# Optimization experiments

Hardware: AMD Instinct MI355X
Metric: run time of the kernel (lower is better)

## Reference

```python
import jax, jax.numpy as jnp
import numpy as np

N, T, F_IN = 20000, 13, 3
E = 320000
NB, NL = 4, 2
C_RES, C_DIL, C_SKIP, C_END = 32, 32, 256, 512
KSZ, KHOP = 2, 4
N_PRED, N_OUT = 12, 2
L = NB * NL
DILS = [2 ** i for _ in range(NB) for i in range(NL)]  # [1,2,1,2,1,2,1,2]
EPS = 1e-5


def _dconv(x, w, d):
    # x: [N,C,T], w: [O,I,K]; valid dilated conv -> [N,O,T-(K-1)*d]
    return jax.lax.conv_general_dilated(x, w, (1,), 'VALID', rhs_dilation=(d,),
                                        dimension_numbers=('NCH', 'OIH', 'NCH'))


def _forward(inputs, edge_src, edge_dst, enter_w, enter_b, filt_w, filt_b, gate_w, gate_b,
             gc_w, gc_b, skip_w, skip_b, bn_g, bn_b, out1_w, out1_b, out2_w, out2_b):
    # inputs: [N,T,F] -> x: [N,C_RES,T] via 1x1 conv (enter)
    x = jnp.einsum('of,ntf->not', enter_w, inputs) + enter_b[None, :, None]
    deg = jax.ops.segment_sum(jnp.ones((E,), x.dtype), edge_dst, num_segments=N)
    deg = jnp.maximum(deg, 1.0)[:, None, None]

    def propagate(h):  # [N,t,C]: mean over incoming edges (normalized diffusion step)
        return jax.ops.segment_sum(h[edge_src], edge_dst, num_segments=N) / deg

    skip = jnp.zeros((N, C_SKIP, T), x.dtype)
    for l in range(L):
        d = DILS[l]
        f = jnp.tanh(_dconv(x, filt_w[l], d) + filt_b[l][None, :, None])
        g = jax.nn.sigmoid(_dconv(x, gate_w[l], d) + gate_b[l][None, :, None])
        h = f * g                                   # [N,C_DIL,t]
        t = h.shape[-1]
        skip = skip[..., -t:] + jnp.einsum('oc,nct->not', skip_w[l], h) + skip_b[l][None, :, None]
        # K-hop graph diffusion conv on [N,t,C]
        hh = h.transpose(0, 2, 1)
        acc = jnp.einsum('ntc,co->nto', hh, gc_w[l, 0])
        cur = hh
        for k in range(1, KHOP):
            cur = propagate(cur)
            acc = acc + jnp.einsum('ntc,co->nto', cur, gc_w[l, k])
        acc = acc + gc_b[l]
        x = acc.transpose(0, 2, 1) + x[..., -t:]    # residual add
        # BatchNorm1d over (N, t) per channel (training-mode batch stats)
        mu = x.mean(axis=(0, 2), keepdims=True)
        var = x.var(axis=(0, 2), keepdims=True)
        x = bn_g[l][None, :, None] * (x - mu) * jax.lax.rsqrt(var + EPS) + bn_b[l][None, :, None]
    y = jax.nn.relu(skip)                           # [N,C_SKIP,1]
    y = jax.nn.relu(jnp.einsum('oc,nct->not', out1_w, y) + out1_b[None, :, None])
    y = jnp.einsum('oc,nct->not', out2_w, y) + out2_b[None, :, None]  # [N,n_pred*n_out,1]
    return y.reshape(N, N_PRED, -1)


def setup_inputs() -> dict:
    key = jax.random.key(0)
    ks = jax.random.split(key, 12)
    s = 0.05
    f32 = jnp.float32
    return {
        'inputs': jax.random.normal(ks[0], (N, T, F_IN), f32),
        'edge_src': jax.random.randint(ks[1], (E,), 0, N),
        'edge_dst': jax.random.randint(ks[2], (E,), 0, N),
        'enter_w': jax.random.normal(ks[3], (C_RES, F_IN), f32) * s,
        'enter_b': jnp.zeros((C_RES,), f32),
        'filt_w': jax.random.normal(ks[4], (L, C_DIL, C_RES, KSZ), f32) * s,
        'filt_b': jnp.zeros((L, C_DIL), f32),
        'gate_w': jax.random.normal(ks[5], (L, C_DIL, C_RES, KSZ), f32) * s,
        'gate_b': jnp.zeros((L, C_DIL), f32),
        'gc_w': jax.random.normal(ks[6], (L, KHOP, C_DIL, C_RES), f32) * s,
        'gc_b': jnp.zeros((L, C_RES), f32),
        'skip_w': jax.random.normal(ks[7], (L, C_SKIP, C_DIL), f32) * s,
        'skip_b': jnp.zeros((L, C_SKIP), f32),
        'bn_g': jnp.ones((L, C_RES), f32),
        'bn_b': jnp.zeros((L, C_RES), f32),
        'out1_w': jax.random.normal(ks[8], (C_END, C_SKIP), f32) * s,
        'out1_b': jnp.zeros((C_END,), f32),
        'out2_w': jax.random.normal(ks[9], (N_PRED * N_OUT, C_END), f32) * s,
        'out2_b': jnp.zeros((N_PRED * N_OUT,), f32),
    }


def reference(inputs, edge_src, edge_dst, enter_w, enter_b, filt_w, filt_b, gate_w, gate_b,
              gc_w, gc_b, skip_w, skip_b, bn_g, bn_b, out1_w, out1_b, out2_w, out2_b):
    return _forward(inputs, edge_src, edge_dst, enter_w, enter_b, filt_w, filt_b, gate_w, gate_b,
                    gc_w, gc_b, skip_w, skip_b, bn_g, bn_b, out1_w, out1_b, out2_w, out2_b)
```

## Files before the change

kernel.cpp:

```cpp
#include <hip/hip_runtime.h>
#include <cmath>

constexpr int N = 20000, T = 13, E = 320000;
constexpr int NB_SCAN = (N + 255) / 256;
constexpr int NPART = 64;
typedef unsigned int uint32;

typedef __attribute__((ext_vector_type(8))) short short8;
typedef __attribute__((ext_vector_type(4))) float f32x4;

__device__ __forceinline__ unsigned short f2bf(float f) {
  unsigned int u = __float_as_uint(f);
  unsigned int r = (u + 0x7FFFu + ((u >> 16) & 1u)) >> 16;
  return (unsigned short)r;
}
__device__ __forceinline__ float bflo(uint32 v) { return __uint_as_float(v << 16); }
__device__ __forceinline__ float bfhi(uint32 v) { return __uint_as_float(v & 0xFFFF0000u); }
__device__ __forceinline__ uint32 packbf(float lo, float hi) {
  return (uint32)f2bf(lo) | ((uint32)f2bf(hi) << 16);
}

constexpr size_t WALIGN = 512;
constexpr size_t align_up(size_t x) { return (x + WALIGN - 1) & ~(WALIGN - 1); }

constexpr size_t XA_OFF  = 0;
constexpr size_t X_SZ    = align_up((size_t)N * 13 * 32 * 4);
constexpr size_t XB_OFF  = XA_OFF + X_SZ;
constexpr size_t H_OFF   = XB_OFF + X_SZ;
constexpr size_t H_SZ    = align_up((size_t)N * 12 * 32 * 4);
constexpr size_t C1_OFF  = H_OFF + H_SZ;
constexpr size_t C2_OFF  = C1_OFF + H_SZ;
constexpr size_t C3_OFF  = C2_OFF + H_SZ;
constexpr size_t HL_OFF  = C3_OFF + H_SZ;
constexpr size_t HL_SZ   = align_up((size_t)N * 256 * 4);
constexpr size_t WS2_OFF = HL_OFF + HL_SZ;
constexpr size_t SB_OFF  = WS2_OFF + align_up(256 * 256 * 4);
constexpr size_t SUMS_OFF = SB_OFF + align_up(256 * 4);
constexpr size_t PAR_OFF  = SUMS_OFF + align_up(8 * NPART * 64 * 4);
constexpr size_t CNT_OFF  = PAR_OFF + align_up(9 * 64 * 4);
constexpr size_t ROW_OFF  = CNT_OFF + align_up((size_t)N * 4);
constexpr size_t FILL_OFF = ROW_OFF + align_up((size_t)(N + 1) * 4);
constexpr size_t COL_OFF  = FILL_OFF + align_up((size_t)N * 4);
constexpr size_t DEG_OFF  = COL_OFF + align_up((size_t)E * 4);
constexpr size_t BP_OFF   = DEG_OFF + align_up((size_t)N * 4);
constexpr size_t CP_OFF   = BP_OFF + align_up(8 * 2048 * 4);
constexpr size_t BW1_OFF  = CP_OFF + align_up(8 * 2176 * 4);
constexpr size_t BW2_OFF  = BW1_OFF + align_up(32768 * 4);
constexpr size_t BS_OFF   = BW2_OFF + align_up(65536 * 4);
constexpr size_t BO_OFF   = BS_OFF + align_up((size_t)NB_SCAN * 4);
constexpr size_t S_OFF  = C2_OFF;
constexpr size_t Y1_OFF = H_OFF;

__global__ void k_count(const int* __restrict__ dst, int* __restrict__ cnt) {
  int i = blockIdx.x * 256 + threadIdx.x;
  if (i < E) atomicAdd(&cnt[dst[i]], 1);
}

__global__ __launch_bounds__(256) void k_scan1(const int* __restrict__ cnt, int* __restrict__ bsum) {
  __shared__ int sc[256];
  int t = threadIdx.x; int idx = blockIdx.x * 256 + t;
  int v = (idx < N) ? cnt[idx] : 0;
  sc[t] = v; __syncthreads();
  for (int off = 1; off < 256; off <<= 1) {
    int u = (t >= off) ? sc[t - off] : 0;
    __syncthreads();
    sc[t] += u;
    __syncthreads();
  }
  if (t == 255) bsum[blockIdx.x] = sc[255];
}

__global__ __launch_bounds__(256) void k_scan2(const int* __restrict__ bsum, int* __restrict__ boff) {
  __shared__ int sc[256];
  int t = threadIdx.x;
  int v = (t < NB_SCAN) ? bsum[t] : 0;
  sc[t] = v; __syncthreads();
  for (int off = 1; off < 256; off <<= 1) {
    int u = (t >= off) ? sc[t - off] : 0;
    __syncthreads();
    sc[t] += u;
    __syncthreads();
  }
  if (t < NB_SCAN) boff[t] = sc[t] - v;
  if (t == 255) boff[NB_SCAN] = sc[255];
}

__global__ __launch_bounds__(256) void k_scan3(const int* __restrict__ cnt, const int* __restrict__ boff,
                                               int* __restrict__ rowptr, int* __restrict__ fill,
                                               float* __restrict__ deginv) {
  __shared__ int sc[256];
  int t = threadIdx.x; int idx = blockIdx.x * 256 + t;
  int v = (idx < N) ? cnt[idx] : 0;
  sc[t] = v; __syncthreads();
  for (int off = 1; off < 256; off <<= 1) {
    int u = (t >= off) ? sc[t - off] : 0;
    __syncthreads();
    sc[t] += u;
    __syncthreads();
  }
  if (idx < N) {
    int run = boff[blockIdx.x] + sc[t] - v;
    rowptr[idx] = run; fill[idx] = run;
    deginv[idx] = 1.0f / (float)(v > 1 ? v : 1);
  }
  if (blockIdx.x == 0 && t == 0) rowptr[N] = boff[NB_SCAN];
}

__global__ void k_scatter(const int* __restrict__ src, const int* __restrict__ dst,
                          int* __restrict__ fill, int* __restrict__ col) {
  int i = blockIdx.x * 256 + threadIdx.x;
  if (i < E) { int d = dst[i]; int p = atomicAdd(&fill[d], 1); col[p] = src[i]; }
}

__global__ void k_init_params(float* __restrict__ par) {
  int i = threadIdx.x;
  par[i] = (i < 32) ? 1.0f : 0.0f;
}

__global__ void k_prep_gcw(const float* __restrict__ gcw, uint32* __restrict__ bp) {
  int idx = blockIdx.x * 256 + threadIdx.x;
  if (idx >= 8 * 4 * 2 * 64 * 4) return;
  int w4 = idx & 3, lane = (idx >> 2) & 63, hh = (idx >> 8) & 1, s = (idx >> 9) & 3, l = idx >> 11;
  int n = lane & 15, q = lane >> 4;
  int k0 = q * 8 + w4 * 2, o = hh * 16 + n;
  const float* g = gcw + (((size_t)(l * 4 + s) * 32 + k0) * 32 + o);
  bp[idx] = packbf(g[0], g[32]);
}

__global__ void k_prep_bw(const float* __restrict__ W, uint32* __restrict__ bp, int O) {
  int idx = blockIdx.x * 256 + threadIdx.x;
  int total = (O / 16) * 8 * 64 * 4;
  if (idx >= total) return;
  int w4 = idx & 3, lane = (idx >> 2) & 63, ks = (idx >> 8) & 7, ot = idx >> 11;
  int n = lane & 15, q = lane >> 4;
  int k = ks * 32 + q * 8 + w4 * 2;
  const float* wr = W + (size_t)(ot * 16 + n) * 256 + k;
  bp[idx] = packbf(wr[0], wr[1]);
}

__global__ void k_prep_conv(const float* __restrict__ fw, const float* __restrict__ fb,
                            const float* __restrict__ gw, const float* __restrict__ gb,
                            const float* __restrict__ par, int layer, uint32* __restrict__ cpbuf) {
  uint32* base = cpbuf + (size_t)layer * 2176;
  int tid = blockIdx.x * 256 + threadIdx.x;
  if (tid < 2048) {
    int w4 = tid & 3, lane = (tid >> 2) & 63, hh = (tid >> 8) & 1, ktap = (tid >> 9) & 1, sel = tid >> 10;
    int n = lane & 15, q = lane >> 4;
    int c0 = q * 8 + w4 * 2, o = hh * 16 + n;
    const float* w = sel ? gw : fw;
    float sc0 = par[layer * 64 + c0], sc1 = par[layer * 64 + c0 + 1];
    float v0 = w[(((size_t)layer * 32 + o) * 32 + c0) * 2 + ktap] * sc0;
    float v1 = w[(((size_t)layer * 32 + o) * 32 + c0 + 1) * 2 + ktap] * sc1;
    base[tid] = packbf(v0, v1);
  } else if (tid < 2048 + 64) {
    int i = tid - 2048; int sel = i >> 5; int o = i & 31;
    const float* w = sel ? gw : fw;
    const float* b = sel ? gb : fb;
    float s = b[layer * 32 + o];
    for (int c = 0; c < 32; c++) {
      float sh = par[layer * 64 + 32 + c];
      s += (w[(((size_t)layer * 32 + o) * 32 + c) * 2 + 0] +
            w[(((size_t)layer * 32 + o) * 32 + c) * 2 + 1]) * sh;
    }
    ((float*)base)[2048 + i] = s;
  }
}

__global__ void k_enter(const float* __restrict__ in, const float* __restrict__ w,
                        const float* __restrict__ b, uint32* __restrict__ x) {
  int idx = blockIdx.x * 256 + threadIdx.x;
  if (idx >= N * 13 * 16) return;
  int cw = idx & 15; int tmp = idx >> 4; int t = tmp % 13; int n = tmp / 13;
  int c0 = cw * 2;
  const float* ip = in + (size_t)n * (13 * 3) + t * 3;
  float v0 = b[c0]     + w[c0 * 3 + 0]       * ip[0] + w[c0 * 3 + 1]       * ip[1] + w[c0 * 3 + 2]       * ip[2];
  float v1 = b[c0 + 1] + w[(c0 + 1) * 3 + 0] * ip[0] + w[(c0 + 1) * 3 + 1] * ip[1] + w[(c0 + 1) * 3 + 2] * ip[2];
  x[idx] = packbf(v0, v1);
}

template <int TIN, int TOUT, int D>
__global__ __launch_bounds__(256, 4) void k_conv(const uint32* __restrict__ x,
    const uint32* __restrict__ cpbuf, int layer,
    uint32* __restrict__ h, float* __restrict__ hlast) {
  constexpr int RS = 34;
  __shared__ float xst[128 * RS];
  int tid = threadIdx.x;
  int wave = tid >> 6, lane = tid & 63;
  int m = lane & 15, q = lane >> 4;
  int nrows = N * TOUT;
  int base = blockIdx.x * 128;

  const uint32* cp = cpbuf + (size_t)layer * 2176;
  short8 bf[2][2][2];
#pragma unroll
  for (int sel = 0; sel < 2; sel++)
#pragma unroll
    for (int kt = 0; kt < 2; kt++)
#pragma unroll
      for (int hh = 0; hh < 2; hh++)
        bf[sel][kt][hh] = *(const short8*)(cp + (size_t)(((sel * 2 + kt) * 2 + hh) * 64 + lane) * 4);
  const float* bias = (const float*)(cp + 2048);
  float fb0 = bias[m], fb1 = bias[16 + m], gb0 = bias[32 + m], gb1 = bias[48 + m];

#pragma unroll
  for (int tile = 0; tile < 2; tile++) {
    int row = base + wave * 32 + tile * 16 + m;
    bool valid = row < nrows;
    int rr = valid ? row : 0;
    int n = rr / TOUT, tt = rr - n * TOUT;
    const uint32* xr = x + ((size_t)n * TIN + tt) * 16 + q * 4;
    short8 a0 = {0,0,0,0,0,0,0,0}, aD = {0,0,0,0,0,0,0,0};
    if (valid) { a0 = *(const short8*)xr; aD = *(const short8*)(xr + D * 16); }
    f32x4 aF0 = {0.f,0.f,0.f,0.f}, aF1 = {0.f,0.f,0.f,0.f};
    f32x4 aG0 = {0.f,0.f,0.f,0.f}, aG1 = {0.f,0.f,0.f,0.f};
    aF0 = __builtin_amdgcn_mfma_f32_16x16x32_bf16(a0, bf[0][0][0], aF0, 0, 0, 0);
    aF0 = __builtin_amdgcn_mfma_f32_16x16x32_bf16(aD, bf[0][1][0], aF0, 0, 0, 0);
    aF1 = __builtin_amdgcn_mfma_f32_16x16x32_bf16(a0, bf[0][0][1], aF1, 0, 0, 0);
    aF1 = __builtin_amdgcn_mfma_f32_16x16x32_bf16(aD, bf[0][1][1], aF1, 0, 0, 0);
    aG0 = __builtin_amdgcn_mfma_f32_16x16x32_bf16(a0, bf[1][0][0], aG0, 0, 0, 0);
    aG0 = __builtin_amdgcn_mfma_f32_16x16x32_bf16(aD, bf[1][1][0], aG0, 0, 0, 0);
    aG1 = __builtin_amdgcn_mfma_f32_16x16x32_bf16(a0, bf[1][0][1], aG1, 0, 0, 0);
    aG1 = __builtin_amdgcn_mfma_f32_16x16x32_bf16(aD, bf[1][1][1], aG1, 0, 0, 0);
#pragma unroll
    for (int r = 0; r < 4; r++) {
      int lrow = wave * 32 + tile * 16 + q * 4 + r;
      float F0 = aF0[r] + fb0, G0 = aG0[r] + gb0;
      float F1 = aF1[r] + fb1, G1 = aG1[r] + gb1;
      float af0 = fabsf(F0), ef0 = __expf(-2.0f * af0);
      float th0 = copysignf((1.0f - ef0) / (1.0f + ef0), F0);
      float hv0 = th0 * (1.0f / (1.0f + __expf(-G0)));
      float af1 = fabsf(F1), ef1 = __expf(-2.0f * af1);
      float th1 = copysignf((1.0f - ef1) / (1.0f + ef1), F1);
      float hv1 = th1 * (1.0f / (1.0f + __expf(-G1)));
      xst[lrow * RS + m]      = hv0;
      xst[lrow * RS + 16 + m] = hv1;
    }
  }
  __syncthreads();
  {
    uint2* outp = (uint2*)h;
#pragma unroll
    for (int it = 0; it < 4; it++) {
      int l = it * 256 + tid;
      int g = base * 8 + l;
      if (g < nrows * 8) {
        int rl = l >> 3, j4 = l & 7;
        float2 a = *(const float2*)&xst[rl * RS + j4 * 4];
        float2 b = *(const float2*)&xst[rl * RS + j4 * 4 + 2];
        outp[g] = make_uint2(packbf(a.x, a.y), packbf(b.x, b.y));
        int grow = base + rl;
        int node = grow / TOUT, tt = grow - node * TOUT;
        if (tt == TOUT - 1) {
          *(float4*)(hlast + (size_t)node * 256 + layer * 32 + j4 * 4) = make_float4(a.x, a.y, b.x, b.y);
        }
      }
    }
  }
}

template <int F>
__global__ __launch_bounds__(256) void k_hop(const uint32* __restrict__ in, uint32* __restrict__ out,
    const int* __restrict__ rowptr, const int* __restrict__ col, const float* __restrict__ deginv) {
  constexpr int F2 = F / 2;
  constexpr int NW = (F2 + 63) / 64;
  int wid = (blockIdx.x * 256 + threadIdx.x) >> 6;
  int lane = threadIdx.x & 63;
  if (wid >= N) return;
  int s = rowptr[wid], e = rowptr[wid + 1];
  float alo[NW], ahi[NW];
#pragma unroll
  for (int k = 0; k < NW; k++) { alo[k] = 0.0f; ahi[k] = 0.0f; }
  int idx = s;
  for (; idx + 7 < e; idx += 8) {
    const uint32* p[8];
#pragma unroll
    for (int q = 0; q < 8; q++) p[q] = in + (size_t)col[idx + q] * F2;
    uint32 v[8][NW];
#pragma unroll
    for (int q = 0; q < 8; q++) {
#pragma unroll
      for (int k = 0; k < NW; k++) {
        int j = k * 64 + lane;
        v[q][k] = (j < F2) ? p[q][j] : 0u;
      }
    }
#pragma unroll
    for (int k = 0; k < NW; k++) {
      alo[k] += ((bflo(v[0][k]) + bflo(v[1][k])) + (bflo(v[2][k]) + bflo(v[3][k]))) +
                ((bflo(v[4][k]) + bflo(v[5][k])) + (bflo(v[6][k]) + bflo(v[7][k])));
      ahi[k] += ((bfhi(v[0][k]) + bfhi(v[1][k])) + (bfhi(v[2][k]) + bfhi(v[3][k]))) +
                ((bfhi(v[4][k]) + bfhi(v[5][k])) + (bfhi(v[6][k]) + bfhi(v[7][k])));
    }
  }
  for (; idx + 3 < e; idx += 4) {
    const uint32* p0 = in + (size_t)col[idx] * F2;
    const uint32* p1 = in + (size_t)col[idx + 1] * F2;
    const uint32* p2 = in + (size_t)col[idx + 2] * F2;
    const uint32* p3 = in + (size_t)col[idx + 3] * F2;
#pragma unroll
    for (int k = 0; k < NW; k++) {
      int j = k * 64 + lane;
      if (j < F2) {
        uint32 v0 = p0[j], v1 = p1[j], v2 = p2[j], v3 = p3[j];
        alo[k] += (bflo(v0) + bflo(v1)) + (bflo(v2) + bflo(v3));
        ahi[k] += (bfhi(v0) + bfhi(v1)) + (bfhi(v2) + bfhi(v3));
      }
    }
  }
  for (; idx < e; ++idx) {
    const uint32* p = in + (size_t)col[idx] * F2;
#pragma unroll
    for (int k = 0; k < NW; k++) {
      int j = k * 64 + lane;
      if (j < F2) { uint32 v = p[j]; alo[k] += bflo(v); ahi[k] += bfhi(v); }
    }
  }
  float inv = deginv[wid];
  uint32* q = out + (size_t)wid * F2;
#pragma unroll
  for (int k = 0; k < NW; k++) {
    int j = k * 64 + lane;
    if (j < F2) q[j] = packbf(alo[k] * inv, ahi[k] * inv);
  }
}

template <int TIN, int TOUT>
__global__ __launch_bounds__(256, 4) void k_combine(const uint32* __restrict__ h,
    const uint32* __restrict__ c1, const uint32* __restrict__ c2, const uint32* __restrict__ c3,
    const uint32* __restrict__ bpack, const float* __restrict__ gcb,
    const uint32* __restrict__ xcur, int layer,
    const float* __restrict__ par, int slot,
    uint32* __restrict__ xnext, float* __restrict__ sums) {
  constexpr int RS = 34;
  __shared__ float xst[128 * RS];
  __shared__ float pbuf[96];
  __shared__ float r1s[32], r2s[32];
  int tid = threadIdx.x;
  if (tid < 32) {
    pbuf[tid]      = gcb[layer * 32 + tid];
    pbuf[32 + tid] = par[slot * 64 + tid];
    pbuf[64 + tid] = par[slot * 64 + 32 + tid];
    r1s[tid] = 0.0f; r2s[tid] = 0.0f;
  }

  int nrows = N * TOUT;
  int base = blockIdx.x * 128;
  int wave = tid >> 6, lane = tid & 63;
  int m = lane & 15, q = lane >> 4;

  const uint32* bp = bpack + (size_t)layer * 2048;
  short8 bf[4][2];
#pragma unroll
  for (int s = 0; s < 4; s++)
#pragma unroll
    for (int hh = 0; hh < 2; hh++)
      bf[s][hh] = *(const short8*)(bp + (size_t)((s * 2 + hh) * 64 + lane) * 4);

  f32x4 acc[2][2] = {{{0.f,0.f,0.f,0.f},{0.f,0.f,0.f,0.f}},{{0.f,0.f,0.f,0.f},{0.f,0.f,0.f,0.f}}};
  const uint32* srcs[4] = { h, c1, c2, c3 };
#pragma unroll
  for (int s = 0; s < 4; s++) {
    const uint32* sp = srcs[s];
#pragma unroll
    for (int t = 0; t < 2; t++) {
      int row = base + wave * 32 + t * 16 + m;
      short8 af = {0,0,0,0,0,0,0,0};
      if (row < nrows) af = *(const short8*)(sp + (size_t)row * 16 + q * 4);
      acc[t][0] = __builtin_amdgcn_mfma_f32_16x16x32_bf16(af, bf[s][0], acc[t][0], 0, 0, 0);
      acc[t][1] = __builtin_amdgcn_mfma_f32_16x16x32_bf16(af, bf[s][1], acc[t][1], 0, 0, 0);
    }
  }

  __syncthreads();
#pragma unroll
  for (int t = 0; t < 2; t++)
#pragma unroll
    for (int hh = 0; hh < 2; hh++)
#pragma unroll
      for (int r = 0; r < 4; r++)
        xst[(wave * 32 + t * 16 + q * 4 + r) * RS + hh * 16 + m] = acc[t][hh][r];
  __syncthreads();

  constexpr int toff = TIN - TOUT;
  int rg = tid >> 3, oq = tid & 7;
  float gb0 = pbuf[oq * 4 + 0], gb1 = pbuf[oq * 4 + 1], gb2 = pbuf[oq * 4 + 2], gb3 = pbuf[oq * 4 + 3];
  float sc0 = pbuf[32 + oq * 4 + 0], sc1 = pbuf[32 + oq * 4 + 1], sc2 = pbuf[32 + oq * 4 + 2], sc3 = pbuf[32 + oq * 4 + 3];
  float sh0 = pbuf[64 + oq * 4 + 0], sh1 = pbuf[64 + oq * 4 + 1], sh2 = pbuf[64 + oq * 4 + 2], sh3 = pbuf[64 + oq * 4 + 3];
  float s1[4] = {0.f, 0.f, 0.f, 0.f}, s2[4] = {0.f, 0.f, 0.f, 0.f};
#pragma unroll
  for (int i = 0; i < 4; i++) {
    int r = rg + 32 * i;
    int row = base + r;
    bool act = row < nrows;
    float2 aa = *(const float2*)&xst[r * RS + oq * 4];
    float2 ab = *(const float2*)&xst[r * RS + oq * 4 + 2];
    float xr0 = 0.f, xr1 = 0.f, xr2 = 0.f, xr3 = 0.f;
    if (act) {
      int node = row / TOUT, t_ = row - node * TOUT;
      const uint32* rp = xcur + ((size_t)node * TIN + toff + t_) * 16 + oq * 2;
      uint32 va = rp[0], vb = rp[1];
      xr0 = bflo(va); xr1 = bfhi(va); xr2 = bflo(vb); xr3 = bfhi(vb);
    }
    float v0 = aa.x + gb0 + sc0 * xr0 + sh0;
    float v1 = aa.y + gb1 + sc1 * xr1 + sh1;
    float v2 = ab.x + gb2 + sc2 * xr2 + sh2;
    float v3 = ab.y + gb3 + sc3 * xr3 + sh3;
    *(float2*)&xst[r * RS + oq * 4]     = make_float2(v0, v1);
    *(float2*)&xst[r * RS + oq * 4 + 2] = make_float2(v2, v3);
    if (act) {
      s1[0] += v0; s1[1] += v1; s1[2] += v2; s1[3] += v3;
      s2[0] += v0 * v0; s2[1] += v1 * v1; s2[2] += v2 * v2; s2[3] += v3 * v3;
    }
  }
#pragma unroll
  for (int j = 0; j < 4; j++) {
    atomicAdd(&r1s[oq * 4 + j], s1[j]);
    atomicAdd(&r2s[oq * 4 + j], s2[j]);
  }
  __syncthreads();

  {
    uint2* outp = (uint2*)xnext;
#pragma unroll
    for (int it = 0; it < 4; it++) {
      int l = it * 256 + tid;
      int g = base * 8 + l;
      if (g < nrows * 8) {
        int rl = l >> 3, j4 = l & 7;
        float2 a = *(const float2*)&xst[rl * RS + j4 * 4];
        float2 b = *(const float2*)&xst[rl * RS + j4 * 4 + 2];
        outp[g] = make_uint2(packbf(a.x, a.y), packbf(b.x, b.y));
      }
    }
  }
  {
    int part = blockIdx.x & (NPART - 1);
    float* sp = sums + ((size_t)layer * NPART + part) * 64;
    if (tid < 32) atomicAdd(&sp[tid], r1s[tid]);
    else if (tid < 64) atomicAdd(&sp[tid], r2s[tid - 32]);
  }
}

__global__ void k_bnfin(const float* __restrict__ sums, const float* __restrict__ bng,
                        const float* __restrict__ bnb, float* __restrict__ par,
                        int layer, int tout) {
  int o = threadIdx.x;
  float cnt = (float)N * (float)tout;
  float s1 = 0.0f, s2 = 0.0f;
  const float* lp = sums + (size_t)layer * NPART * 64;
  for (int p = 0; p < NPART; p++) {
    s1 += lp[p * 64 + o];
    s2 += lp[p * 64 + 32 + o];
  }
  float mu = s1 / cnt;
  float var = s2 / cnt - mu * mu;
  float sc = bng[layer * 32 + o] * rsqrtf(var + 1e-5f);
  par[(layer + 1) * 64 + o] = sc;
  par[(layer + 1) * 64 + 32 + o] = bnb[layer * 32 + o] - mu * sc;
}

__global__ void k_prep_skipw(const float* __restrict__ sw, float* __restrict__ w2) {
  int idx = blockIdx.x * 256 + threadIdx.x;
  if (idx >= 8 * 256 * 32) return;
  int l = idx / (256 * 32), r = idx % (256 * 32), o = r / 32, c = r & 31;
  w2[o * 256 + l * 32 + c] = sw[idx];
}
__global__ void k_prep_sb(const float* __restrict__ sb, float* __restrict__ out) {
  int o = threadIdx.x;
  float s = 0.0f;
  for (int l = 0; l < 8; l++) s += sb[l * 256 + o];
  out[o] = s;
}

__global__ __launch_bounds__(256) void k_mgemm(const float* __restrict__ A, const uint32* __restrict__ bp,
    const float* __restrict__ bias, float* __restrict__ C, int M, int Onum, int relu) {
  constexpr int RS = 68;
  __shared__ float xst[128 * RS];
  int tid = threadIdx.x;
  int wave = tid >> 6, lane = tid & 63;
  int m = lane & 15, q = lane >> 4;
  int base = blockIdx.x * 128;
  int ot0 = blockIdx.y * 4;

  f32x4 acc[2][4];
#pragma unroll
  for (int t = 0; t < 2; t++)
#pragma unroll
    for (int nt = 0; nt < 4; nt++) acc[t][nt] = (f32x4){0.f, 0.f, 0.f, 0.f};

#pragma unroll 1
  for (int ks = 0; ks < 8; ks++) {
    short8 a[2];
#pragma unroll
    for (int t = 0; t < 2; t++) {
      int row = base + wave * 32 + t * 16 + m;
      float4 f0 = make_float4(0.f, 0.f, 0.f, 0.f), f1 = f0;
      if (row < M) {
        const float* ap = A + (size_t)row * 256 + ks * 32 + q * 8;
        f0 = *(const float4*)ap;
        f1 = *(const float4*)(ap + 4);
      }
      uint32 u[4];
      u[0] = packbf(f0.x, f0.y); u[1] = packbf(f0.z, f0.w);
      u[2] = packbf(f1.x, f1.y); u[3] = packbf(f1.z, f1.w);
      a[t] = *(const short8*)u;
    }
#pragma unroll
    for (int nt = 0; nt < 4; nt++) {
      short8 b = *(const short8*)(bp + (size_t)(((ot0 + nt) * 8 + ks) * 64 + lane) * 4);
      acc[0][nt] = __builtin_amdgcn_mfma_f32_16x16x32_bf16(a[0], b, acc[0][nt], 0, 0, 0);
      acc[1][nt] = __builtin_amdgcn_mfma_f32_16x16x32_bf16(a[1], b, acc[1][nt], 0, 0, 0);
    }
  }

#pragma unroll
  for (int t = 0; t < 2; t++)
#pragma unroll
    for (int nt = 0; nt < 4; nt++) {
      float bv = bias[blockIdx.y * 64 + nt * 16 + m];
#pragma unroll
      for (int r = 0; r < 4; r++) {
        float v = acc[t][nt][r] + bv;
        if (relu) v = fmaxf(v, 0.0f);
        xst[(wave * 32 + t * 16 + q * 4 + r) * RS + nt * 16 + m] = v;
      }
    }
  __syncthreads();

#pragma unroll
  for (int it = 0; it < 8; it++) {
    int l = it * 256 + tid;
    int rl = l >> 4, c4 = l & 15;
    int grow = base + rl;
    if (grow < M) {
      float4 v = *(const float4*)&xst[rl * RS + c4 * 4];
      *(float4*)(C + (size_t)grow * Onum + blockIdx.y * 64 + c4 * 4) = v;
    }
  }
}

__global__ __launch_bounds__(256) void k_final2(const float* __restrict__ Y1, const float* __restrict__ W2,
                                                const float* __restrict__ b2, float* __restrict__ out) {
  __shared__ float y1s[64][68];
  __shared__ float w2s[24][65];
  int tid = threadIdx.x;
  int bm = blockIdx.x * 64;
  int k0 = blockIdx.y * 64;
  for (int i = tid; i < 64 * 16; i += 256) {
    int r = i >> 4, k4 = i & 15;
    int gm = bm + r;
    float4 v = make_float4(0.f, 0.f, 0.f, 0.f);
    if (gm < N) v = *(const float4*)(Y1 + (size_t)gm * 512 + k0 + k4 * 4);
    y1s[r][k4 * 4 + 0] = v.x; y1s[r][k4 * 4 + 1] = v.y;
    y1s[r][k4 * 4 + 2] = v.z; y1s[r][k4 * 4 + 3] = v.w;
  }
  for (int i = tid; i < 24 * 16; i += 256) {
    int o = i >> 4, k4 = i & 15;
    float4 v = *(const float4*)(W2 + (size_t)o * 512 + k0 + k4 * 4);
    w2s[o][k4 * 4 + 0] = v.x; w2s[o][k4 * 4 + 1] = v.y;
    w2s[o][k4 * 4 + 2] = v.z; w2s[o][k4 * 4 + 3] = v.w;
  }
  __syncthreads();
  int rg = tid >> 5;
  int o = tid & 31;
  if (o < 24) {
    float acc[8] = {};
    for (int kk = 0; kk < 64; kk++) {
      float w = w2s[o][kk];
#pragma unroll
      for (int i = 0; i < 8; i++) acc[i] += y1s[rg * 8 + i][kk] * w;
    }
    float bias = (blockIdx.y == 0) ? b2[o] : 0.0f;
#pragma unroll
    for (int i = 0; i < 8; i++) {
      int gm = bm + rg * 8 + i;
      if (gm < N) atomicAdd(&out[(size_t)gm * 24 + o], acc[i] + bias);
    }
  }
}

struct Ptrs {
  const float *fw, *fb, *gw, *gb, *gcb, *bng, *bnb;
  const uint32 *bpack;
  uint32 *cpack;
  void *H, *C1, *C2, *C3;
  float *HL, *par, *sums;
  const int *row, *col;
  const float *deg;
};

template <int TIN, int TOUT, int D>
static void run_layer(int layer, bool last, const Ptrs& P, uint32*& xc, uint32*& xn, hipStream_t stream) {
  int cblocks = (N * TOUT + 127) / 128;
  k_conv<TIN, TOUT, D><<<cblocks, 256, 0, stream>>>(xc, P.cpack, layer, (uint32*)P.H, P.HL);
  if (!last) {
    constexpr int F = TOUT * 32;
    int hb = (N * 64 + 255) / 256;
    k_hop<F><<<hb, 256, 0, stream>>>((const uint32*)P.H, (uint32*)P.C1, P.row, P.col, P.deg);
    k_hop<F><<<hb, 256, 0, stream>>>((const uint32*)P.C1, (uint32*)P.C2, P.row, P.col, P.deg);
    k_hop<F><<<hb, 256, 0, stream>>>((const uint32*)P.C2, (uint32*)P.C3, P.row, P.col, P.deg);
    k_combine<TIN, TOUT><<<cblocks, 256, 0, stream>>>((const uint32*)P.H, (const uint32*)P.C1,
                                                      (const uint32*)P.C2, (const uint32*)P.C3,
                                                      P.bpack, P.gcb, xc, layer, P.par, layer, xn, P.sums);
    k_bnfin<<<1, 32, 0, stream>>>(P.sums, P.bng, P.bnb, P.par, layer, TOUT);
    k_prep_conv<<<9, 256, 0, stream>>>(P.fw, P.fb, P.gw, P.gb, P.par, layer + 1, P.cpack);
    uint32* tmp = xc; xc = xn; xn = tmp;
  }
}

extern "C" void kernel_launch(void* const* d_in, const int* in_sizes, int n_in,
                              void* d_out, int out_size, void* d_ws, size_t ws_size,
                              hipStream_t stream) {
  const float* inputs  = (const float*)d_in[0];
  const int*   esrc    = (const int*)d_in[1];
  const int*   edst    = (const int*)d_in[2];
  const float* enter_w = (const float*)d_in[3];
  const float* enter_b = (const float*)d_in[4];
  const float* filt_w  = (const float*)d_in[5];
  const float* filt_b  = (const float*)d_in[6];
  const float* gate_w  = (const float*)d_in[7];
  const float* gate_b  = (const float*)d_in[8];
  const float* gc_w    = (const float*)d_in[9];
  const float* gc_b    = (const float*)d_in[10];
  const float* skip_w  = (const float*)d_in[11];
  const float* skip_b  = (const float*)d_in[12];
  const float* bn_g    = (const float*)d_in[13];
  const float* bn_b    = (const float*)d_in[14];
  const float* out1_w  = (const float*)d_in[15];
  const float* out1_b  = (const float*)d_in[16];
  const float* out2_w  = (const float*)d_in[17];
  const float* out2_b  = (const float*)d_in[18];

  char* ws = (char*)d_ws;
  uint32* XA = (uint32*)(ws + XA_OFF);
  uint32* XB = (uint32*)(ws + XB_OFF);
  void* H    = (void*)(ws + H_OFF);
  void* C1   = (void*)(ws + C1_OFF);
  void* C2   = (void*)(ws + C2_OFF);
  void* C3   = (void*)(ws + C3_OFF);
  float* HL  = (float*)(ws + HL_OFF);
  float* WS2 = (float*)(ws + WS2_OFF);
  float* SB  = (float*)(ws + SB_OFF);
  float* SUMS = (float*)(ws + SUMS_OFF);
  float* PAR  = (float*)(ws + PAR_OFF);
  int* CNT  = (int*)(ws + CNT_OFF);
  int* ROW  = (int*)(ws + ROW_OFF);
  int* FILL = (int*)(ws + FILL_OFF);
  int* COL  = (int*)(ws + COL_OFF);
  float* DEG = (float*)(ws + DEG_OFF);
  uint32* BP = (uint32*)(ws + BP_OFF);
  uint32* CP = (uint32*)(ws + CP_OFF);
  uint32* BW1 = (uint32*)(ws + BW1_OFF);
  uint32* BW2 = (uint32*)(ws + BW2_OFF);
  int* BS = (int*)(ws + BS_OFF);
  int* BO = (int*)(ws + BO_OFF);
  float* S  = (float*)(ws + S_OFF);
  float* Y1 = (float*)(ws + Y1_OFF);

  hipMemsetAsync(CNT, 0, (size_t)N * 4, stream);
  hipMemsetAsync(SUMS, 0, (size_t)8 * NPART * 64 * 4, stream);
  hipMemsetAsync(d_out, 0, (size_t)out_size * 4, stream);

  k_count<<<(E + 255) / 256, 256, 0, stream>>>(edst, CNT);
  k_scan1<<<NB_SCAN, 256, 0, stream>>>(CNT, BS);
  k_scan2<<<1, 256, 0, stream>>>(BS, BO);
  k_scan3<<<NB_SCAN, 256, 0, stream>>>(CNT, BO, ROW, FILL, DEG);
  k_scatter<<<(E + 255) / 256, 256, 0, stream>>>(esrc, edst, FILL, COL);
  k_init_params<<<1, 64, 0, stream>>>(PAR);
  k_prep_gcw<<<(8 * 4 * 2 * 64 * 4 + 255) / 256, 256, 0, stream>>>(gc_w, BP);
  k_prep_conv<<<9, 256, 0, stream>>>(filt_w, filt_b, gate_w, gate_b, PAR, 0, CP);
  k_enter<<<(N * 13 * 16 + 255) / 256, 256, 0, stream>>>(inputs, enter_w, enter_b, XA);
  k_prep_skipw<<<(8 * 256 * 32 + 255) / 256, 256, 0, stream>>>(skip_w, WS2);
  k_prep_sb<<<1, 256, 0, stream>>>(skip_b, SB);
  k_prep_bw<<<(32768 + 255) / 256, 256, 0, stream>>>(WS2, BW1, 256);
  k_prep_bw<<<(65536 + 255) / 256, 256, 0, stream>>>(out1_w, BW2, 512);

  Ptrs P;
  P.fw = filt_w; P.fb = filt_b; P.gw = gate_w; P.gb = gate_b;
  P.gcb = gc_b; P.bng = bn_g; P.bnb = bn_b; P.bpack = BP; P.cpack = CP;
  P.H = H; P.C1 = C1; P.C2 = C2; P.C3 = C3; P.HL = HL; P.par = PAR; P.sums = SUMS;
  P.row = ROW; P.col = COL; P.deg = DEG;

  uint32* xc = XA; uint32* xn = XB;
  run_layer<13, 12, 1>(0, false, P, xc, xn, stream);
  run_layer<12, 10, 2>(1, false, P, xc, xn, stream);
  run_layer<10, 9, 1>(2, false, P, xc, xn, stream);
  run_layer<9, 7, 2>(3, false, P, xc, xn, stream);
  run_layer<7, 6, 1>(4, false, P, xc, xn, stream);
  run_layer<6, 4, 2>(5, false, P, xc, xn, stream);
  run_layer<4, 3, 1>(6, false, P, xc, xn, stream);
  run_layer<3, 1, 2>(7, true, P, xc, xn, stream);

  dim3 g1((N + 127) / 128, 4);
  k_mgemm<<<g1, 256, 0, stream>>>(HL, BW1, SB, S, N, 256, 1);
  dim3 g2((N + 127) / 128, 8);
  k_mgemm<<<g2, 256, 0, stream>>>(S, BW2, out1_b, Y1, N, 512, 1);
  dim3 gf((N + 63) / 64, 8);
  k_final2<<<gf, 256, 0, stream>>>(Y1, out2_w, out2_b, (float*)d_out);
}
```

Before: 1.018 ms.

## Fuse output head GEMMs with bf16 intermediates and MFMA final projection

Stores the last-step hidden features and the skip GEMM output in bf16 rather than fp32, so the A operands load directly as MFMA fragments without conversion. The second head GEMM is fused with the final 512->24 projection via MFMA on the ReLU'd tile in shared memory. This removes the fp32 Y1 intermediate and the separate scalar k_final2 kernel. Each block now computes 8 output tiles instead of 4, which raises register use, and the final outputs are still summed with atomics across column blocks.

```diff
diff --git a/kernel.cpp b/kernel.cpp
--- a/kernel.cpp
+++ b/kernel.cpp
@@ -49,7 +49,6 @@
 constexpr size_t BS_OFF   = BW2_OFF + align_up(65536 * 4);
 constexpr size_t BO_OFF   = BS_OFF + align_up((size_t)NB_SCAN * 4);
 constexpr size_t S_OFF  = C2_OFF;
-constexpr size_t Y1_OFF = H_OFF;
 
 __global__ void k_count(const int* __restrict__ dst, int* __restrict__ cnt) {
   int i = blockIdx.x * 256 + threadIdx.x;
@@ -136,6 +135,18 @@
   int k = ks * 32 + q * 8 + w4 * 2;
   const float* wr = W + (size_t)(ot * 16 + n) * 256 + k;
   bp[idx] = packbf(wr[0], wr[1]);
+}
+
+__global__ void k_prep_w2(const float* __restrict__ W, uint32* __restrict__ bp) {
+  int idx = blockIdx.x * 256 + threadIdx.x;
+  if (idx >= 2 * 16 * 64 * 4) return;
+  int w4 = idx & 3, lane = (idx >> 2) & 63, ks = (idx >> 8) & 15, ot = idx >> 12;
+  int n = lane & 15, q = lane >> 4;
+  int k = ks * 32 + q * 8 + w4 * 2;
+  int o = ot * 16 + n;
+  float v0 = 0.0f, v1 = 0.0f;
+  if (o < 24) { const float* wr = W + (size_t)o * 512 + k; v0 = wr[0]; v1 = wr[1]; }
+  bp[idx] = packbf(v0, v1);
 }
 
 __global__ void k_prep_conv(const float* __restrict__ fw, const float* __restrict__ fb,
@@ -181,7 +192,7 @@
 template <int TIN, int TOUT, int D>
 __global__ __launch_bounds__(256, 4) void k_conv(const uint32* __restrict__ x,
     const uint32* __restrict__ cpbuf, int layer,
-    uint32* __restrict__ h, float* __restrict__ hlast) {
+    uint32* __restrict__ h, uint32* __restrict__ hlast) {
   constexpr int RS = 34;
   __shared__ float xst[128 * RS];
   int tid = threadIdx.x;
@@ -247,11 +258,12 @@
         int rl = l >> 3, j4 = l & 7;
         float2 a = *(const float2*)&xst[rl * RS + j4 * 4];
         float2 b = *(const float2*)&xst[rl * RS + j4 * 4 + 2];
-        outp[g] = make_uint2(packbf(a.x, a.y), packbf(b.x, b.y));
+        uint2 pv = make_uint2(packbf(a.x, a.y), packbf(b.x, b.y));
+        outp[g] = pv;
         int grow = base + rl;
         int node = grow / TOUT, tt = grow - node * TOUT;
         if (tt == TOUT - 1) {
-          *(float4*)(hlast + (size_t)node * 256 + layer * 32 + j4 * 4) = make_float4(a.x, a.y, b.x, b.y);
+          *(uint2*)(hlast + (size_t)node * 128 + layer * 16 + j4 * 2) = pv;
         }
       }
     }
@@ -472,111 +484,160 @@
   out[o] = s;
 }
 
-__global__ __launch_bounds__(256) void k_mgemm(const float* __restrict__ A, const uint32* __restrict__ bp,
-    const float* __restrict__ bias, float* __restrict__ C, int M, int Onum, int relu) {
+__global__ __launch_bounds__(256) void k_gemm1(const uint32* __restrict__ A,
+    const uint32* __restrict__ bp, const float* __restrict__ bias, uint32* __restrict__ Sb) {
   constexpr int RS = 68;
   __shared__ float xst[128 * RS];
   int tid = threadIdx.x;
   int wave = tid >> 6, lane = tid & 63;
   int m = lane & 15, q = lane >> 4;
   int base = blockIdx.x * 128;
-  int ot0 = blockIdx.y * 4;
-
-  f32x4 acc[2][4];
+  int ot0 = blockIdx.y * 8;
+
+  f32x4 acc[2][8];
 #pragma unroll
   for (int t = 0; t < 2; t++)
 #pragma unroll
-    for (int nt = 0; nt < 4; nt++) acc[t][nt] = (f32x4){0.f, 0.f, 0.f, 0.f};
-
+    for (int nt = 0; nt < 8; nt++) acc[t][nt] = (f32x4){0.f, 0.f, 0.f, 0.f};
+
+  int row0 = base + wave * 32 + m;
+  int row1 = row0 + 16;
 #pragma unroll 1
   for (int ks = 0; ks < 8; ks++) {
-    short8 a[2];
-#pragma unroll
-    for (int t = 0; t < 2; t++) {
-      int row = base + wave * 32 + t * 16 + m;
-      float4 f0 = make_float4(0.f, 0.f, 0.f, 0.f), f1 = f0;
-      if (row < M) {
-        const float* ap = A + (size_t)row * 256 + ks * 32 + q * 8;
-        f0 = *(const float4*)ap;
-        f1 = *(const float4*)(ap + 4);
-      }
-      uint32 u[4];
-      u[0] = packbf(f0.x, f0.y); u[1] = packbf(f0.z, f0.w);
-      u[2] = packbf(f1.x, f1.y); u[3] = packbf(f1.z, f1.w);
-      a[t] = *(const short8*)u;
-    }
-#pragma unroll
-    for (int nt = 0; nt < 4; nt++) {
+    short8 a0 = {0,0,0,0,0,0,0,0}, a1 = {0,0,0,0,0,0,0,0};
+    if (row0 < N) a0 = *(const short8*)(A + (size_t)row0 * 128 + ks * 16 + q * 4);
+    if (row1 < N) a1 = *(const short8*)(A + (size_t)row1 * 128 + ks * 16 + q * 4);
+#pragma unroll
+    for (int nt = 0; nt < 8; nt++) {
       short8 b = *(const short8*)(bp + (size_t)(((ot0 + nt) * 8 + ks) * 64 + lane) * 4);
-      acc[0][nt] = __builtin_amdgcn_mfma_f32_16x16x32_bf16(a[0], b, acc[0][nt], 0, 0, 0);
-      acc[1][nt] = __builtin_amdgcn_mfma_f32_16x16x32_bf16(a[1], b, acc[1][nt], 0, 0, 0);
-    }
-  }
-
+      acc[0][nt] = __builtin_amdgcn_mfma_f32_16x16x32_bf16(a0, b, acc[0][nt], 0, 0, 0);
+      acc[1][nt] = __builtin_amdgcn_mfma_f32_16x16x32_bf16(a1, b, acc[1][nt], 0, 0, 0);
+    }
+  }
+
+#pragma unroll
+  for (int half = 0; half < 2; half++) {
+    if (half) __syncthreads();
+#pragma unroll
+    for (int t = 0; t < 2; t++)
+#pragma unroll
+      for (int nn = 0; nn < 4; nn++) {
+        float bv = bias[blockIdx.y * 128 + (half * 4 + nn) * 16 + m];
+#pragma unroll
+        for (int r = 0; r < 4; r++) {
+          float v = acc[t][half * 4 + nn][r] + bv;
+          xst[(wave * 32 + t * 16 + q * 4 + r) * RS + nn * 16 + m] = fmaxf(v, 0.0f);
+        }
+      }
+    __syncthreads();
+#pragma unroll
+    for (int it = 0; it < 8; it++) {
+      int l = it * 256 + tid;
+      int rl = l >> 4, c4 = l & 15;
+      int grow = base + rl;
+      if (grow < N) {
+        float2 a = *(const float2*)&xst[rl * RS + c4 * 4];
+        float2 b = *(const float2*)&xst[rl * RS + c4 * 4 + 2];
+        *(uint2*)(Sb + (size_t)grow * 128 + blockIdx.y * 64 + half * 32 + c4 * 2) =
+            make_uint2(packbf(a.x, a.y), packbf(b.x, b.y));
+      }
+    }
+  }
+}
+
+__global__ __launch_bounds__(256) void k_gemm2f(const uint32* __restrict__ A,
+    const uint32* __restrict__ bp, const float* __restrict__ bias,
+    const uint32* __restrict__ w2p, const float* __restrict__ b2, float* __restrict__ out) {
+  constexpr int RS = 68;
+  __shared__ float xst[128 * RS];
+  int tid = threadIdx.x;
+  int wave = tid >> 6, lane = tid & 63;
+  int m = lane & 15, q = lane >> 4;
+  int base = blockIdx.x * 128;
+  int ot0 = blockIdx.y * 8;
+
+  f32x4 acc[2][8];
 #pragma unroll
   for (int t = 0; t < 2; t++)
 #pragma unroll
-    for (int nt = 0; nt < 4; nt++) {
-      float bv = bias[blockIdx.y * 64 + nt * 16 + m];
-#pragma unroll
-      for (int r = 0; r < 4; r++) {
-        float v = acc[t][nt][r] + bv;
-        if (relu) v = fmaxf(v, 0.0f);
-        xst[(wave * 32 + t * 16 + q * 4 + r) * RS + nt * 16 + m] = v;
-      }
-    }
-  __syncthreads();
-
-#pragma unroll
-  for (int it = 0; it < 8; it++) {
-    int l = it * 256 + tid;
-    int rl = l >> 4, c4 = l & 15;
-    int grow = base + rl;
-    if (grow < M) {
-      float4 v = *(const float4*)&xst[rl * RS + c4 * 4];
-      *(float4*)(C + (size_t)grow * Onum + blockIdx.y * 64 + c4 * 4) = v;
-    }
-  }
-}
-
-__global__ __launch_bounds__(256) void k_final2(const float* __restrict__ Y1, const float* __restrict__ W2,
-                                                const float* __restrict__ b2, float* __restrict__ out) {
-  __shared__ float y1s[64][68];
-  __shared__ float w2s[24][65];
-  int tid = threadIdx.x;
-  int bm = blockIdx.x * 64;
-  int k0 = blockIdx.y * 64;
-  for (int i = tid; i < 64 * 16; i += 256) {
-    int r = i >> 4, k4 = i & 15;
-    int gm = bm + r;
-    float4 v = make_float4(0.f, 0.f, 0.f, 0.f);
-    if (gm < N) v = *(const float4*)(Y1 + (size_t)gm * 512 + k0 + k4 * 4);
-    y1s[r][k4 * 4 + 0] = v.x; y1s[r][k4 * 4 + 1] = v.y;
-    y1s[r][k4 * 4 + 2] = v.z; y1s[r][k4 * 4 + 3] = v.w;
-  }
-  for (int i = tid; i < 24 * 16; i += 256) {
-    int o = i >> 4, k4 = i & 15;
-    float4 v = *(const float4*)(W2 + (size_t)o * 512 + k0 + k4 * 4);
-    w2s[o][k4 * 4 + 0] = v.x; w2s[o][k4 * 4 + 1] = v.y;
-    w2s[o][k4 * 4 + 2] = v.z; w2s[o][k4 * 4 + 3] = v.w;
-  }
-  __syncthreads();
-  int rg = tid >> 5;
-  int o = tid & 31;
-  if (o < 24) {
-    float acc[8] = {};
-    for (int kk = 0; kk < 64; kk++) {
-      float w = w2s[o][kk];
-#pragma unroll
-      for (int i = 0; i < 8; i++) acc[i] += y1s[rg * 8 + i][kk] * w;
-    }
-    float bias = (blockIdx.y == 0) ? b2[o] : 0.0f;
-#pragma unroll
-    for (int i = 0; i < 8; i++) {
-      int gm = bm + rg * 8 + i;
-      if (gm < N) atomicAdd(&out[(size_t)gm * 24 + o], acc[i] + bias);
-    }
-  }
+    for (int nt = 0; nt < 8; nt++) acc[t][nt] = (f32x4){0.f, 0.f, 0.f, 0.f};
+
+  int row0 = base + wave * 32 + m;
+  int row1 = row0 + 16;
+#pragma unroll 1
+  for (int ks = 0; ks < 8; ks++) {
+    short8 a0 = {0,0,0,0,0,0,0,0}, a1 = {0,0,0,0,0,0,0,0};
+    if (row0 < N) a0 = *(const short8*)(A + (size_t)row0 * 128 + ks * 16 + q * 4);
+    if (row1 < N) a1 = *(const short8*)(A + (size_t)row1 * 128 + ks * 16 + q * 4);
+#pragma unroll
+    for (int nt = 0; nt < 8; nt++) {
+      short8 b = *(const short8*)(bp + (size_t)(((ot0 + nt) * 8 + ks) * 64 + lane) * 4);
+      acc[0][nt] = __builtin_amdgcn_mfma_f32_16x16x32_bf16(a0, b, acc[0][nt], 0, 0, 0);
+      acc[1][nt] = __builtin_amdgcn_mfma_f32_16x16x32_bf16(a1, b, acc[1][nt], 0, 0, 0);
+    }
+  }
+
+  f32x4 acc2[2][2];
+#pragma unroll
+  for (int t = 0; t < 2; t++)
+#pragma unroll
+    for (int o2 = 0; o2 < 2; o2++) acc2[t][o2] = (f32x4){0.f, 0.f, 0.f, 0.f};
+
+#pragma unroll
+  for (int half = 0; half < 2; half++) {
+    if (half) __syncthreads();
+#pragma unroll
+    for (int t = 0; t < 2; t++)
+#pragma unroll
+      for (int nn = 0; nn < 4; nn++) {
+        float bv = bias[blockIdx.y * 128 + (half * 4 + nn) * 16 + m];
+#pragma unroll
+        for (int r = 0; r < 4; r++) {
+          float v = acc[t][half * 4 + nn][r] + bv;
+          xst[(wave * 32 + t * 16 + q * 4 + r) * RS + nn * 16 + m] = fmaxf(v, 0.0f);
+        }
+      }
+    __syncthreads();
+#pragma unroll
+    for (int kl = 0; kl < 2; kl++) {
+      short8 a2[2];
+#pragma unroll
+      for (int t = 0; t < 2; t++) {
+        const float* xp = &xst[(size_t)(wave * 32 + t * 16 + m) * RS + kl * 32 + q * 8];
+        float4 f0 = *(const float4*)xp;
+        float4 f1 = *(const float4*)(xp + 4);
+        uint32 u[4];
+        u[0] = packbf(f0.x, f0.y); u[1] = packbf(f0.z, f0.w);
+        u[2] = packbf(f1.x, f1.y); u[3] = packbf(f1.z, f1.w);
+        a2[t] = *(const short8*)u;
+      }
+      int ksg = blockIdx.y * 4 + half * 2 + kl;
+#pragma unroll
+      for (int o2 = 0; o2 < 2; o2++) {
+        short8 b = *(const short8*)(w2p + (size_t)(((o2 * 16 + ksg) * 64 + lane) * 4));
+        acc2[0][o2] = __builtin_amdgcn_mfma_f32_16x16x32_bf16(a2[0], b, acc2[0][o2], 0, 0, 0);
+        acc2[1][o2] = __builtin_amdgcn_mfma_f32_16x16x32_bf16(a2[1], b, acc2[1][o2], 0, 0, 0);
+      }
+    }
+  }
+
+#pragma unroll
+  for (int t = 0; t < 2; t++)
+#pragma unroll
+    for (int o2 = 0; o2 < 2; o2++) {
+      int oc = o2 * 16 + m;
+      if (oc < 24) {
+#pragma unroll
+        for (int r = 0; r < 4; r++) {
+          int row = base + wave * 32 + t * 16 + q * 4 + r;
+          if (row < N) {
+            float v = acc2[t][o2][r];
+            if (blockIdx.y == 0) v += b2[oc];
+            atomicAdd(&out[(size_t)row * 24 + oc], v);
+          }
+        }
+      }
+    }
 }
 
 struct Ptrs {
@@ -584,7 +645,8 @@
   const uint32 *bpack;
   uint32 *cpack;
   void *H, *C1, *C2, *C3;
-  float *HL, *par, *sums;
+  uint32 *HL;
+  float *par, *sums;
   const int *row, *col;
   const float *deg;
 };
@@ -638,7 +700,7 @@
   void* C1   = (void*)(ws + C1_OFF);
   void* C2   = (void*)(ws + C2_OFF);
   void* C3   = (void*)(ws + C3_OFF);
-  float* HL  = (float*)(ws + HL_OFF);
+  uint32* HLB = (uint32*)(ws + HL_OFF);
   float* WS2 = (float*)(ws + WS2_OFF);
   float* SB  = (float*)(ws + SB_OFF);
   float* SUMS = (float*)(ws + SUMS_OFF);
@@ -654,8 +716,8 @@
   uint32* BW2 = (uint32*)(ws + BW2_OFF);
   int* BS = (int*)(ws + BS_OFF);
   int* BO = (int*)(ws + BO_OFF);
-  float* S  = (float*)(ws + S_OFF);
-  float* Y1 = (float*)(ws + Y1_OFF);
+  uint32* Sb  = (uint32*)(ws + S_OFF);
+  uint32* W2P = (uint32*)(ws + WS2_OFF);
 
   hipMemsetAsync(CNT, 0, (size_t)N * 4, stream);
   hipMemsetAsync(SUMS, 0, (size_t)8 * NPART * 64 * 4, stream);
@@ -674,11 +736,12 @@
   k_prep_sb<<<1, 256, 0, stream>>>(skip_b, SB);
   k_prep_bw<<<(32768 + 255) / 256, 256, 0, stream>>>(WS2, BW1, 256);
   k_prep_bw<<<(65536 + 255) / 256, 256, 0, stream>>>(out1_w, BW2, 512);
+  k_prep_w2<<<(8192 + 255) / 256, 256, 0, stream>>>(out2_w, W2P);
 
   Ptrs P;
   P.fw = filt_w; P.fb = filt_b; P.gw = gate_w; P.gb = gate_b;
   P.gcb = gc_b; P.bng = bn_g; P.bnb = bn_b; P.bpack = BP; P.cpack = CP;
-  P.H = H; P.C1 = C1; P.C2 = C2; P.C3 = C3; P.HL = HL; P.par = PAR; P.sums = SUMS;
+  P.H = H; P.C1 = C1; P.C2 = C2; P.C3 = C3; P.HL = HLB; P.par = PAR; P.sums = SUMS;
   P.row = ROW; P.col = COL; P.deg = DEG;
 
   uint32* xc = XA; uint32* xn = XB;
@@ -691,10 +754,8 @@
   run_layer<4, 3, 1>(6, false, P, xc, xn, stream);
   run_layer<3, 1, 2>(7, true, P, xc, xn, stream);
 
-  dim3 g1((N + 127) / 128, 4);
-  k_mgemm<<<g1, 256, 0, stream>>>(HL, BW1, SB, S, N, 256, 1);
-  dim3 g2((N + 127) / 128, 8);
-  k_mgemm<<<g2, 256, 0, stream>>>(S, BW2, out1_b, Y1, N, 512, 1);
-  dim3 gf((N + 63) / 64, 8);
-  k_final2<<<gf, 256, 0, stream>>>(Y1, out2_w, out2_b, (float*)d_out);
-}
+  dim3 g1((N + 127) / 128, 2);
+  k_gemm1<<<g1, 256, 0, stream>>>(HLB, BW1, SB, Sb);
+  dim3 g2((N + 127) / 128, 4);
+  k_gemm2f<<<g2, 256, 0, stream>>>(Sb, BW2, out1_b, W2P, out2_b, (float*)d_out);
+}
```

After: 974.0 us. 1.05x faster.
